# Kernel optimization log

Hardware: AMD Instinct MI355X
Metric: run time of the kernel (lower is better)

## Reference

```python
import jax, jax.numpy as jnp
import numpy as np

C = 80           # foreground classes
B, N = 8, 4000   # images, proposals per image
K_PRE = 2048     # pre-NMS candidates per image (fixed-shape stand-in for torch.where filtering)
DET = 100        # detection_per_image
SCORE_THRESH = 0.01
NMS_THRESH = 0.5
MIN_AREA = 0.1
BBOX_W = (10.0, 10.0, 5.0, 5.0)
CLIP = float(np.log(1000.0 / 16.0))
CLS_OFFSET = 4096.0               # > max image coordinate, for batched (per-class) NMS


def setup_inputs() -> dict:
    key = jax.random.key(0)
    k1, k2, k3, k4 = jax.random.split(key, 4)
    p1 = jax.random.uniform(k1, (B, N, 2)) * 800.0
    wh = jax.random.uniform(k2, (B, N, 2)) * 200.0 + 1.0
    proposals = jnp.concatenate([p1, p1 + wh], axis=-1)          # [B,N,4] x1,y1,x2,y2
    label_pre = jax.random.normal(k3, (B, N, C + 1), dtype=jnp.float32)
    bbox_pre = jax.random.normal(k4, (B, N, (C + 1) * 4), dtype=jnp.float32) * 0.5
    return {"label_pre": label_pre, "bbox_pre": bbox_pre, "proposals": proposals}


def decode_boxes(deltas, props):
    w = props[..., 2] - props[..., 0]
    h = props[..., 3] - props[..., 1]
    cx = props[..., 0] + 0.5 * w
    cy = props[..., 1] + 0.5 * h
    dx = deltas[..., 0] / BBOX_W[0]
    dy = deltas[..., 1] / BBOX_W[1]
    dw = jnp.minimum(deltas[..., 2] / BBOX_W[2], CLIP)
    dh = jnp.minimum(deltas[..., 3] / BBOX_W[3], CLIP)
    pcx = dx * w + cx
    pcy = dy * h + cy
    pw = jnp.exp(dw) * w
    ph = jnp.exp(dh) * h
    return jnp.stack([pcx - 0.5 * pw, pcy - 0.5 * ph,
                      pcx + 0.5 * pw, pcy + 0.5 * ph], axis=-1)


def pairwise_iou(b):
    # b [K,4] -> [K,K]
    area = jnp.maximum(b[:, 2] - b[:, 0], 0.0) * jnp.maximum(b[:, 3] - b[:, 1], 0.0)
    lt = jnp.maximum(b[:, None, :2], b[None, :, :2])
    rb = jnp.minimum(b[:, None, 2:], b[None, :, 2:])
    wh = jnp.maximum(rb - lt, 0.0)
    inter = wh[..., 0] * wh[..., 1]
    union = area[:, None] + area[None, :] - inter
    return inter / jnp.maximum(union, 1e-9)


def greedy_nms_keep(boxes, valid):
    # boxes already sorted by score (descending); returns kept mask
    K = boxes.shape[0]
    iou = pairwise_iou(boxes)
    idx = jnp.arange(K)

    def body(i, keep):
        sup = (iou[i] > NMS_THRESH) & (idx > i) & keep[i]
        return keep & ~sup

    return jax.lax.fori_loop(0, K, body, valid)


def process_image(logits, deltas, props):
    probs = jax.nn.softmax(logits, axis=-1)            # [N, C+1]
    scores = probs[:, 1:].reshape(-1)                  # [N*C]
    d = deltas[:, 4:].reshape(N, C, 4)                 # drop background deltas
    boxes = decode_boxes(d, props[:, None, :]).reshape(-1, 4)   # [N*C, 4]
    labels = jnp.broadcast_to(jnp.arange(1, C + 1), (N, C)).reshape(-1)
    area = (boxes[:, 3] - boxes[:, 1]) * (boxes[:, 2] - boxes[:, 0])
    valid = (scores > SCORE_THRESH) & (area > MIN_AREA)
    masked = jnp.where(valid, scores, -1.0)
    top_scores, top_idx = jax.lax.top_k(masked, K_PRE)
    top_boxes = boxes[top_idx]
    top_labels = labels[top_idx]
    keep0 = top_scores > 0.0
    # batched_nms: per-class coordinate offset so classes never suppress each other
    off = (top_labels.astype(top_boxes.dtype) * CLS_OFFSET)[:, None]
    keep = greedy_nms_keep(top_boxes + off, keep0)
    final = jnp.where(keep, top_scores, -1.0)
    det_scores, det_idx = jax.lax.top_k(final, DET)
    return top_boxes[det_idx], det_scores, top_labels[det_idx]


def reference(label_pre, bbox_pre, proposals):
    # returns (boxes [B,DET,4], scores [B,DET], labels [B,DET]); entries with score<0 are padding
    return jax.vmap(process_image)(label_pre, bbox_pre, proposals)
```

## Files before the change

### kernel.cpp

```cpp
#include <hip/hip_runtime.h>
#include <stdint.h>

#define B_ 8
#define N_ 4000
#define C_ 80
#define NC_ (N_ * C_)
#define KP_ 2048
#define CAND_ 4096
#define SLOTS_ 32
#define SLOTCAP_ 128
#define DET_ 100
#define NW_ 32
#define CLIP_ 4.135166556742356f

#define PB_ 80
#define IB_ (N_ / PB_)
#define CB_ 64
#define FB_ 128
#define NBLK_ ((NC_ / 4 + 255) / 256)

#define RT_ 256
#define RI_ 4
#define RJS_ 16
#define RSL_ (CAND_ / RJS_)
#define RIB_ (CAND_ / (RT_ * RI_))
#define IBK_ (CAND_ / 256)

typedef unsigned long long u64;

__device__ __forceinline__ void decode4(const float4 pr, const float4 d,
                                        float& x1, float& y1, float& x2, float& y2) {
  float w = pr.z - pr.x, h = pr.w - pr.y;
  float cx = pr.x + 0.5f * w, cy = pr.y + 0.5f * h;
  float dx = d.x / 10.0f, dy = d.y / 10.0f;
  float dw = fminf(d.z / 5.0f, CLIP_), dh = fminf(d.w / 5.0f, CLIP_);
  float pcx = dx * w + cx, pcy = dy * h + cy;
  float pw = expf(dw) * w, ph = expf(dh) * h;
  x1 = pcx - 0.5f * pw; y1 = pcy - 0.5f * ph;
  x2 = pcx + 0.5f * pw; y2 = pcy + 0.5f * ph;
}

__global__ __launch_bounds__(256) void k_scores(const float* __restrict__ logits,
                                                uint32_t* __restrict__ keys,
                                                uint32_t* __restrict__ imgHist) {
  __shared__ float lds[PB_ * 81];
  __shared__ float mArr[PB_], dArr[PB_];
  __shared__ uint32_t hcnt[CB_];
  int blk = blockIdx.x;
  int b = blk / IB_, lb = blk - b * IB_;
  int p0 = b * N_ + lb * PB_;
  int t = threadIdx.x;
  if (t < CB_) hcnt[t] = 0;
  const float4* src = (const float4*)(logits + (size_t)p0 * 81);
  for (int k = t; k < PB_ * 81 / 4; k += 256) ((float4*)lds)[k] = src[k];
  __syncthreads();
  if (t < PB_) {
    const float* lp = lds + t * 81;
    float m = lp[0];
    for (int i = 1; i <= C_; ++i) m = fmaxf(m, lp[i]);
    float denom = 0.f;
    for (int i = 0; i <= C_; ++i) denom += expf(lp[i] - m);
    mArr[t] = m; dArr[t] = denom;
  }
  __syncthreads();
#pragma unroll
  for (int iter = 0; iter < PB_ * C_ / 256; ++iter) {
    int e = iter * 256 + t;
    int pp = e / C_, c = e - pp * C_;
    float lv = lds[pp * 81 + c + 1];
    float score = expf(lv - mArr[pp]) / dArr[pp];
    uint32_t key = 0;
    if (score > 0.01f) {
      key = __float_as_uint(score);
      atomicAdd(&hcnt[(key >> 20) - 960], 1u);
    }
    keys[(size_t)p0 * C_ + e] = key;
  }
  __syncthreads();
  if (t < CB_ && hcnt[t]) atomicAdd(&imgHist[b * CB_ + t], hcnt[t]);
}

__global__ __launch_bounds__(256) void k_refine(const uint32_t* __restrict__ keys,
                                                const uint32_t* __restrict__ imgHist,
                                                uint32_t* __restrict__ fineHist) {
  __shared__ int s_cb;
  int blk = blockIdx.x;
  int b = blk / NBLK_, lb = blk - b * NBLK_;
  int t = threadIdx.x;
  if (t < 64) {
    uint32_t v = imgHist[b * CB_ + t];
#pragma unroll
    for (int d = 1; d < 64; d <<= 1) {
      uint32_t o = __shfl_down(v, d);
      v += (t + d < 64) ? o : 0;
    }
    uint32_t nxt = __shfl_down(v, 1);
    if (t == 63) nxt = 0;
    uint32_t total = __shfl(v, 0);
    if (t == 0 && total < KP_) s_cb = -1;
    if (total >= KP_ && v >= KP_ && nxt < KP_) s_cb = t;
  }
  __syncthreads();
  int cb = s_cb;
  if (cb < 0) return;
  int ti = lb * 256 + t;
  if (ti >= NC_ / 4) return;
  uint4 k4 = ((const uint4*)(keys + (size_t)b * NC_))[ti];
  uint32_t want = (uint32_t)(cb + 960);
  uint32_t kv[4] = {k4.x, k4.y, k4.z, k4.w};
#pragma unroll
  for (int q = 0; q < 4; ++q)
    if ((kv[q] >> 20) == want)
      atomicAdd(&fineHist[b * FB_ + ((kv[q] >> 13) & (FB_ - 1))], 1u);
}

__global__ __launch_bounds__(256) void k_compact(const uint32_t* __restrict__ keys,
                                                 const uint32_t* __restrict__ imgHist,
                                                 const uint32_t* __restrict__ fineHist,
                                                 uint32_t* __restrict__ cnt,
                                                 u64* __restrict__ cand) {
  __shared__ int s_cb;
  __shared__ uint32_t s_tail;
  __shared__ uint32_t s_thr;
  int blk = blockIdx.x;
  int b = blk / NBLK_, lb = blk - b * NBLK_;
  int t = threadIdx.x;
  if (t < 64) {
    uint32_t v = imgHist[b * CB_ + t];
#pragma unroll
    for (int d = 1; d < 64; d <<= 1) {
      uint32_t o = __shfl_down(v, d);
      v += (t + d < 64) ? o : 0;
    }
    uint32_t nxt = __shfl_down(v, 1);
    if (t == 63) nxt = 0;
    uint32_t total = __shfl(v, 0);
    if (t == 0 && total < KP_) { s_cb = -1; s_tail = 0; }
    if (total >= KP_ && v >= KP_ && nxt < KP_) { s_cb = t; s_tail = nxt; }
  }
  __syncthreads();
  int cb = s_cb;
  if (cb < 0) {
    if (t == 0) s_thr = 1u;
  } else if (t < 64) {
    uint32_t f0 = fineHist[b * FB_ + 2 * t];
    uint32_t f1 = fineHist[b * FB_ + 2 * t + 1];
    uint32_t v = f0 + f1;
#pragma unroll
    for (int d = 1; d < 64; d <<= 1) {
      uint32_t o = __shfl_down(v, d);
      v += (t + d < 64) ? o : 0;
    }
    uint32_t nxt = __shfl_down(v, 1);
    if (t == 63) nxt = 0;
    uint32_t tail = s_tail;
    bool c0 = (tail + v >= KP_);
    bool c1 = (tail + nxt + f1 >= KP_);
    bool cN = (tail + nxt >= KP_);
    if (c0 && !c1) s_thr = ((uint32_t)(cb + 960) << 20) | ((uint32_t)(2 * t) << 13);
    if (c1 && !cN) s_thr = ((uint32_t)(cb + 960) << 20) | ((uint32_t)(2 * t + 1) << 13);
  }
  __syncthreads();
  uint32_t thrb = s_thr;
  int ti = lb * 256 + t;
  if (ti >= NC_ / 4) return;
  uint4 k4 = ((const uint4*)(keys + (size_t)b * NC_))[ti];
  int slot = (ti >> 4) & (SLOTS_ - 1);
  uint32_t kv[4] = {k4.x, k4.y, k4.z, k4.w};
  int ns = 0;
#pragma unroll
  for (int q = 0; q < 4; ++q) ns += (kv[q] >= thrb) ? 1 : 0;
  if (ns == 0) return;
  uint32_t pos = atomicAdd(&cnt[(b * SLOTS_ + slot) * 16], (uint32_t)ns);
  u64* seg = cand + (size_t)b * CAND_ + slot * SLOTCAP_;
  uint32_t baseIdx = (uint32_t)(ti * 4);
#pragma unroll
  for (int q = 0; q < 4; ++q) {
    if (kv[q] >= thrb) {
      if (pos < SLOTCAP_)
        seg[pos] = ((u64)kv[q] << 32) | (uint32_t)(~(baseIdx + q));
      ++pos;
    }
  }
}

__global__ __launch_bounds__(256) void k_rank(const u64* __restrict__ cand,
                                              uint32_t* __restrict__ rankPart) {
  __shared__ u64 sh[RSL_];
  int blk = blockIdx.x;
  int b = blk / (RIB_ * RJS_);
  int rem = blk - b * (RIB_ * RJS_);
  int lb = rem / RJS_, js = rem - lb * RJS_;
  int t = threadIdx.x;
  const u64* cb2 = cand + (size_t)b * CAND_;
  if (t < RSL_ / 2)
    ((ulonglong2*)sh)[t] = ((const ulonglong2*)(cb2 + js * RSL_))[t];
  int base = lb * (RT_ * RI_) + t;
  u64 ki[RI_];
#pragma unroll
  for (int q = 0; q < RI_; ++q) ki[q] = cb2[base + q * RT_];
  __syncthreads();
  int cnt[RI_] = {0, 0, 0, 0};
#pragma unroll 4
  for (int j2 = 0; j2 < RSL_ / 2; ++j2) {
    ulonglong2 v = ((const ulonglong2*)sh)[j2];
#pragma unroll
    for (int q = 0; q < RI_; ++q) {
      cnt[q] += (v.x > ki[q]) ? 1 : 0;
      cnt[q] += (v.y > ki[q]) ? 1 : 0;
    }
  }
  uint32_t* rp = rankPart + ((size_t)(b * RJS_ + js)) * CAND_ + base;
#pragma unroll
  for (int q = 0; q < RI_; ++q) rp[q * RT_] = (uint32_t)cnt[q];
}

__global__ __launch_bounds__(256) void k_scatter(
    const u64* __restrict__ cand, const uint32_t* __restrict__ rankPart,
    const float* __restrict__ bbox, const float* __restrict__ props,
    float* __restrict__ topScore, int* __restrict__ topLabel,
    float* __restrict__ topBox, float* __restrict__ nmsBox) {
  int blk = blockIdx.x;
  int b = blk / IBK_, lb = blk - b * IBK_;
  int t = threadIdx.x;
  int i = lb * 256 + t;
  u64 ki = cand[(size_t)b * CAND_ + i];
  if (ki == 0ull) return;
  uint32_t r = 0;
#pragma unroll
  for (int js = 0; js < RJS_; ++js)
    r += rankPart[((size_t)(b * RJS_ + js)) * CAND_ + i];
  if (r >= KP_) return;
  uint32_t sbits = (uint32_t)(ki >> 32);
  uint32_t idx = ~((uint32_t)ki);
  int n = idx / C_, c = idx % C_;
  float4 pr4 = ((const float4*)props)[(size_t)b * N_ + n];
  float4 d = ((const float4*)(bbox + ((size_t)b * N_ + n) * ((C_ + 1) * 4)))[c + 1];
  float x1, y1, x2, y2;
  decode4(pr4, d, x1, y1, x2, y2);
  float off = (float)(c + 1) * 4096.0f;
  size_t o = (size_t)b * KP_ + (size_t)r;
  topScore[o] = __uint_as_float(sbits);
  topLabel[o] = c + 1;
  ((float4*)topBox)[o] = make_float4(x1, y1, x2, y2);
  ((float4*)nmsBox)[o] = make_float4(x1 + off, y1 + off, x2 + off, y2 + off);
}

__global__ __launch_bounds__(64) void k_supmat(const float* __restrict__ nmsBox,
                                               u64* __restrict__ sup) {
  int blk = blockIdx.x;
  int b = blk / 528, r = blk - b * 528;
  int ti = 0, rem = r;
  while (rem >= 32 - ti) { rem -= 32 - ti; ++ti; }
  int tj = ti + rem;
  __shared__ float4 shj[64];
  __shared__ float sha[64];
  int l = threadIdx.x;
  const float4* boxes = (const float4*)(nmsBox + (size_t)b * KP_ * 4);
  float4 bj0 = boxes[tj * 64 + l];
  shj[l] = bj0;
  sha[l] = fmaxf(bj0.z - bj0.x, 0.f) * fmaxf(bj0.w - bj0.y, 0.f);
  int i = ti * 64 + l;
  float4 bi = boxes[i];
  float areai = fmaxf(bi.z - bi.x, 0.f) * fmaxf(bi.w - bi.y, 0.f);
  __syncthreads();
  u64 bits = 0;
  for (int jj = 0; jj < 64; ++jj) {
    int j = tj * 64 + jj;
    if (j > i) {
      float4 bj = shj[jj];
      float ltx = fmaxf(bi.x, bj.x), lty = fmaxf(bi.y, bj.y);
      float rbx = fminf(bi.z, bj.z), rby = fminf(bi.w, bj.w);
      float iw = fmaxf(rbx - ltx, 0.f), ih = fmaxf(rby - lty, 0.f);
      float inter = iw * ih;
      float uni = areai + sha[jj] - inter;
      float iou = inter / fmaxf(uni, 1e-9f);
      if (iou > 0.5f) bits |= (1ull << jj);
    }
  }
  sup[((size_t)b * KP_ + i) * NW_ + tj] = bits;
}

__global__ __launch_bounds__(64) void k_nms_scan(const u64* __restrict__ sup,
                                                 const float* __restrict__ topScore,
                                                 const int* __restrict__ topLabel,
                                                 const float* __restrict__ topBox,
                                                 float* __restrict__ out) {
  int b = blockIdx.x, l = threadIdx.x;
  int h = l >> 5, w = l & 31;
  const u64* base = sup + (size_t)b * KP_ * NW_;
  const float* ts = topScore + (size_t)b * KP_;
  const int* tl = topLabel + (size_t)b * KP_;
  const float4* tb = (const float4*)(topBox + (size_t)b * KP_ * 4);
  unsigned m32 = 0;
#pragma unroll
  for (int j = 0; j < 8; ++j) {
    float4 s4 = ((const float4*)ts)[l * 8 + j];
    if (!(s4.x > 0.f)) m32 |= 1u << (4 * j + 0);
// ... 47 lines not shown
      emitRow(c * 64 + k, true);
    }
    if (outCount >= DET_) return true;
    unsigned kmask = h ? ~rmh : ~rml;
    u64 acc = 0;
#pragma unroll
    for (int k = 0; k < 32; ++k)
      acc |= ((kmask >> k) & 1u) ? cur[k] : 0ull;
    acc |= __shfl_xor(acc, 32);
    removed = (l == c) ? rmfull : removed;
    if (l < 32 && l >= c) removed |= acc;
    return false;
  };

  bool done = false;
  loadc(ra, 0);
  for (int c = 0; c < NW_ && !done; c += 2) {
    if (c + 1 < NW_) loadc(rb, c + 1);
    done = chunk(ra, c);
    if (!done) {
      if (c + 2 < NW_) loadc(ra, c + 2);
      done = chunk(rb, c + 1);
    }
  }
  if (outCount < DET_) {
    for (int c2 = 0; c2 < NW_ && outCount < DET_; ++c2) {
      u64 rm = __shfl(removed, c2);
      while (rm && outCount < DET_) {
        int k = __builtin_ctzll(rm);
        rm &= rm - 1;
        emitRow(c2 * 64 + k, false);
      }
    }
  }
}

extern "C" void kernel_launch(void* const* d_in, const int* in_sizes, int n_in,
                              void* d_out, int out_size, void* d_ws, size_t ws_size,
                              hipStream_t stream) {
  const float* label_pre = (const float*)d_in[0];
  const float* bbox_pre = (const float*)d_in[1];
  const float* props = (const float*)d_in[2];
  float* out = (float*)d_out;

  char* ws = (char*)d_ws;
  size_t off = 0;
  auto alloc = [&](size_t bytes) -> void* {
    void* p = ws + off;
    off = (off + bytes + 255) & ~(size_t)255;
    return p;
  };

  uint32_t* keys = (uint32_t*)alloc((size_t)B_ * NC_ * 4);
  size_t zero_begin = off;
  uint32_t* imgHist = (uint32_t*)alloc((size_t)B_ * CB_ * 4);
  uint32_t* fineHist = (uint32_t*)alloc((size_t)B_ * FB_ * 4);
  uint32_t* cnt = (uint32_t*)alloc((size_t)B_ * SLOTS_ * 16 * 4);
  u64* cand = (u64*)alloc((size_t)B_ * CAND_ * 8);
  float* topScore = (float*)alloc((size_t)B_ * KP_ * 4);
  int* topLabel = (int*)alloc((size_t)B_ * KP_ * 4);
  float* topBox = (float*)alloc((size_t)B_ * KP_ * 16);
  float* nmsBox = (float*)alloc((size_t)B_ * KP_ * 16);
  size_t zero_end = off;
  u64* sup = (u64*)alloc((size_t)B_ * KP_ * NW_ * 8);
  uint32_t* rankPart = (uint32_t*)alloc((size_t)B_ * RJS_ * CAND_ * 4);

  if (off > ws_size) return;

  hipMemsetAsync(ws + zero_begin, 0, zero_end - zero_begin, stream);

  k_scores<<<B_ * IB_, 256, 0, stream>>>(label_pre, keys, imgHist);
  k_refine<<<B_ * NBLK_, 256, 0, stream>>>(keys, imgHist, fineHist);
  k_compact<<<B_ * NBLK_, 256, 0, stream>>>(keys, imgHist, fineHist, cnt, cand);
  k_rank<<<B_ * RIB_ * RJS_, RT_, 0, stream>>>(cand, rankPart);
  k_scatter<<<B_ * IBK_, 256, 0, stream>>>(cand, rankPart, bbox_pre, props,
                                           topScore, topLabel, topBox, nmsBox);
  k_supmat<<<B_ * 528, 64, 0, stream>>>(nmsBox, sup);
  k_nms_scan<<<B_, 64, 0, stream>>>(sup, topScore, topLabel, topBox, out);
}
```

Measured before the change: 183.7 us.

## Fuse all pipeline stages into one cooperative persistent kernel with grid syncs

Replaces the memset plus seven separate kernel launches with a single cooperative kernel of 512 blocks that runs each stage in turn, separated by grid-wide barriers. Zeroing of the workspace happens inside the kernel. The goal is to remove per-launch overhead and the gaps between dependent kernels. In exchange, each stage is limited to the fixed grid, and the supmat and refine/compact stages become grid-stride loops. Grid syncs have their own cost, and if the cooperative launch fails the old multi-kernel path runs instead.

```diff
diff --git a/kernel.cpp b/kernel.cpp
--- a/kernel.cpp
+++ b/kernel.cpp
@@ -1,5 +1,8 @@
 #include <hip/hip_runtime.h>
+#include <hip/hip_cooperative_groups.h>
 #include <stdint.h>
+
+namespace cg = cooperative_groups;
 
 #define B_ 8
 #define N_ 4000
@@ -26,6 +29,8 @@
 #define RIB_ (CAND_ / (RT_ * RI_))
 #define IBK_ (CAND_ / 256)
 
+#define GB_ 512
+
 typedef unsigned long long u64;
 
 __device__ __forceinline__ void decode4(const float4 pr, const float4 d,
@@ -38,6 +43,358 @@
   float pw = expf(dw) * w, ph = expf(dh) * h;
   x1 = pcx - 0.5f * pw; y1 = pcy - 0.5f * ph;
   x2 = pcx + 0.5f * pw; y2 = pcy + 0.5f * ph;
+}
+
+struct SmScores { float lds[PB_ * 81]; float mArr[PB_]; float dArr[PB_]; uint32_t hcnt[CB_]; };
+struct SmSel { int s_cb; uint32_t s_tail; uint32_t s_thr; };
+struct SmSup { float4 shj[4][64]; float sha[4][64]; };
+union SmAll { SmScores sc; SmSel sel; u64 rk[RSL_]; SmSup sup; };
+
+__global__ __launch_bounds__(256, 2) void k_mega(
+    const float* __restrict__ logits, const float* __restrict__ bbox,
+    const float* __restrict__ props,
+    uint32_t* __restrict__ keys, uint32_t* __restrict__ imgHist,
+    uint32_t* __restrict__ fineHist, uint32_t* __restrict__ cnt,
+    u64* __restrict__ cand, float* __restrict__ topScore,
+    int* __restrict__ topLabel, float* __restrict__ topBox,
+    float* __restrict__ nmsBox, u64* __restrict__ sup,
+    uint32_t* __restrict__ rankPart, float* __restrict__ out,
+    uint4* __restrict__ zeroPtr, int zeroN4) {
+  cg::grid_group grid = cg::this_grid();
+  __shared__ SmAll sm;
+  int bid = blockIdx.x, t = threadIdx.x;
+
+  for (int i = bid * 256 + t; i < zeroN4; i += GB_ * 256)
+    zeroPtr[i] = make_uint4(0u, 0u, 0u, 0u);
+  grid.sync();
+
+  if (bid < B_ * IB_) {
+    int b = bid / IB_, lb = bid - b * IB_;
+    int p0 = b * N_ + lb * PB_;
+    if (t < CB_) sm.sc.hcnt[t] = 0;
+    const float4* src = (const float4*)(logits + (size_t)p0 * 81);
+    for (int k = t; k < PB_ * 81 / 4; k += 256) ((float4*)sm.sc.lds)[k] = src[k];
+    __syncthreads();
+    if (t < PB_) {
+      const float* lp = sm.sc.lds + t * 81;
+      float m = lp[0];
+      for (int i = 1; i <= C_; ++i) m = fmaxf(m, lp[i]);
+      float denom = 0.f;
+      for (int i = 0; i <= C_; ++i) denom += expf(lp[i] - m);
+      sm.sc.mArr[t] = m; sm.sc.dArr[t] = denom;
+    }
+    __syncthreads();
+#pragma unroll
+    for (int iter = 0; iter < PB_ * C_ / 256; ++iter) {
+      int e = iter * 256 + t;
+      int pp = e / C_, c = e - pp * C_;
+      float lv = sm.sc.lds[pp * 81 + c + 1];
+      float score = expf(lv - sm.sc.mArr[pp]) / sm.sc.dArr[pp];
+      uint32_t key = 0;
+      if (score > 0.01f) {
+        key = __float_as_uint(score);
+        atomicAdd(&sm.sc.hcnt[(key >> 20) - 960], 1u);
+      }
+      keys[(size_t)p0 * C_ + e] = key;
+    }
+    __syncthreads();
+    if (t < CB_ && sm.sc.hcnt[t]) atomicAdd(&imgHist[b * CB_ + t], sm.sc.hcnt[t]);
+  }
+  grid.sync();
+
+  for (int vb = bid; vb < B_ * NBLK_; vb += GB_) {
+    __syncthreads();
+    int b = vb / NBLK_, lb = vb - b * NBLK_;
+    if (t < 64) {
+      uint32_t v = imgHist[b * CB_ + t];
+#pragma unroll
+      for (int d = 1; d < 64; d <<= 1) {
+        uint32_t o = __shfl_down(v, d);
+        v += (t + d < 64) ? o : 0;
+      }
+      uint32_t nxt = __shfl_down(v, 1);
+      if (t == 63) nxt = 0;
+      uint32_t total = __shfl(v, 0);
+      if (t == 0 && total < KP_) sm.sel.s_cb = -1;
+      if (total >= KP_ && v >= KP_ && nxt < KP_) sm.sel.s_cb = t;
+    }
+    __syncthreads();
+    int cb = sm.sel.s_cb;
+    if (cb >= 0) {
+      int ti = lb * 256 + t;
+      if (ti < NC_ / 4) {
+        uint4 k4 = ((const uint4*)(keys + (size_t)b * NC_))[ti];
+        uint32_t want = (uint32_t)(cb + 960);
+        uint32_t kv[4] = {k4.x, k4.y, k4.z, k4.w};
+#pragma unroll
+        for (int q = 0; q < 4; ++q)
+          if ((kv[q] >> 20) == want)
+            atomicAdd(&fineHist[b * FB_ + ((kv[q] >> 13) & (FB_ - 1))], 1u);
+      }
+    }
+  }
+  grid.sync();
+
+  for (int vb = bid; vb < B_ * NBLK_; vb += GB_) {
+    __syncthreads();
+    int b = vb / NBLK_, lb = vb - b * NBLK_;
+    if (t < 64) {
+      uint32_t v = imgHist[b * CB_ + t];
+#pragma unroll
+      for (int d = 1; d < 64; d <<= 1) {
+        uint32_t o = __shfl_down(v, d);
+        v += (t + d < 64) ? o : 0;
+      }
+      uint32_t nxt = __shfl_down(v, 1);
+      if (t == 63) nxt = 0;
+      uint32_t total = __shfl(v, 0);
+      if (t == 0 && total < KP_) { sm.sel.s_cb = -1; sm.sel.s_tail = 0; }
+      if (total >= KP_ && v >= KP_ && nxt < KP_) { sm.sel.s_cb = t; sm.sel.s_tail = nxt; }
+    }
+    __syncthreads();
+    int cb = sm.sel.s_cb;
+    if (cb < 0) {
+      if (t == 0) sm.sel.s_thr = 1u;
+    } else if (t < 64) {
+      uint32_t f0 = fineHist[b * FB_ + 2 * t];
+      uint32_t f1 = fineHist[b * FB_ + 2 * t + 1];
+      uint32_t v = f0 + f1;
+#pragma unroll
+      for (int d = 1; d < 64; d <<= 1) {
+        uint32_t o = __shfl_down(v, d);
+        v += (t + d < 64) ? o : 0;
+      }
+      uint32_t nxt = __shfl_down(v, 1);
+      if (t == 63) nxt = 0;
+      uint32_t tail = sm.sel.s_tail;
+      bool c0 = (tail + v >= KP_);
+      bool c1 = (tail + nxt + f1 >= KP_);
+      bool cN = (tail + nxt >= KP_);
+      if (c0 && !c1) sm.sel.s_thr = ((uint32_t)(cb + 960) << 20) | ((uint32_t)(2 * t) << 13);
+      if (c1 && !cN) sm.sel.s_thr = ((uint32_t)(cb + 960) << 20) | ((uint32_t)(2 * t + 1) << 13);
+    }
+    __syncthreads();
+    uint32_t thrb = sm.sel.s_thr;
+    int ti = lb * 256 + t;
+    if (ti < NC_ / 4) {
+      uint4 k4 = ((const uint4*)(keys + (size_t)b * NC_))[ti];
+      int slot = (ti >> 4) & (SLOTS_ - 1);
+      uint32_t kv[4] = {k4.x, k4.y, k4.z, k4.w};
+      int ns = 0;
+#pragma unroll
+      for (int q = 0; q < 4; ++q) ns += (kv[q] >= thrb) ? 1 : 0;
+      if (ns != 0) {
+        uint32_t pos = atomicAdd(&cnt[(b * SLOTS_ + slot) * 16], (uint32_t)ns);
+        u64* seg = cand + (size_t)b * CAND_ + slot * SLOTCAP_;
+        uint32_t baseIdx = (uint32_t)(ti * 4);
+#pragma unroll
+        for (int q = 0; q < 4; ++q) {
+          if (kv[q] >= thrb) {
+            if (pos < SLOTCAP_)
+              seg[pos] = ((u64)kv[q] << 32) | (uint32_t)(~(baseIdx + q));
+            ++pos;
+          }
+        }
+      }
+    }
+  }
+  grid.sync();
+
+  {
+    int b = bid / (RIB_ * RJS_);
+    int rem = bid - b * (RIB_ * RJS_);
+    int lb = rem / RJS_, js = rem - lb * RJS_;
+    const u64* cb2 = cand + (size_t)b * CAND_;
+    if (t < RSL_ / 2)
+      ((ulonglong2*)sm.rk)[t] = ((const ulonglong2*)(cb2 + js * RSL_))[t];
+    int base = lb * (RT_ * RI_) + t;
+    u64 ki[RI_];
+#pragma unroll
+    for (int q = 0; q < RI_; ++q) ki[q] = cb2[base + q * RT_];
+    __syncthreads();
+    int cnt4[RI_] = {0, 0, 0, 0};
+#pragma unroll 4
+    for (int j2 = 0; j2 < RSL_ / 2; ++j2) {
+      ulonglong2 v = ((const ulonglong2*)sm.rk)[j2];
+#pragma unroll
+      for (int q = 0; q < RI_; ++q) {
+        cnt4[q] += (v.x > ki[q]) ? 1 : 0;
+        cnt4[q] += (v.y > ki[q]) ? 1 : 0;
+      }
+    }
+    uint32_t* rp = rankPart + ((size_t)(b * RJS_ + js)) * CAND_ + base;
+#pragma unroll
+    for (int q = 0; q < RI_; ++q) rp[q * RT_] = (uint32_t)cnt4[q];
+  }
+  grid.sync();
+
+  if (bid < B_ * IBK_) {
+    int b = bid / IBK_, lb = bid - b * IBK_;
+    int i = lb * 256 + t;
+    u64 ki = cand[(size_t)b * CAND_ + i];
+    if (ki != 0ull) {
+      uint32_t r = 0;
+#pragma unroll
+      for (int js = 0; js < RJS_; ++js)
+        r += rankPart[((size_t)(b * RJS_ + js)) * CAND_ + i];
+      if (r < KP_) {
+        uint32_t sbits = (uint32_t)(ki >> 32);
+        uint32_t idx = ~((uint32_t)ki);
+        int n = idx / C_, c = idx % C_;
+        float4 pr4 = ((const float4*)props)[(size_t)b * N_ + n];
+        float4 d = ((const float4*)(bbox + ((size_t)b * N_ + n) * ((C_ + 1) * 4)))[c + 1];
+        float x1, y1, x2, y2;
+        decode4(pr4, d, x1, y1, x2, y2);
+        float off = (float)(c + 1) * 4096.0f;
+        size_t o = (size_t)b * KP_ + (size_t)r;
+        topScore[o] = __uint_as_float(sbits);
+        topLabel[o] = c + 1;
+        ((float4*)topBox)[o] = make_float4(x1, y1, x2, y2);
+        ((float4*)nmsBox)[o] = make_float4(x1 + off, y1 + off, x2 + off, y2 + off);
+      }
+    }
+  }
+  grid.sync();
+
+  {
+    int l = t & 63, wv = t >> 6;
+    for (int pass = 0; pass < (B_ * 528 + GB_ * 4 - 1) / (GB_ * 4); ++pass) {
+      int tt = pass * GB_ * 4 + bid * 4 + wv;
+      bool act = tt < B_ * 528;
+      int b = 0, tj = 0, i = 0;
+      float4 bi = make_float4(0.f, 0.f, 0.f, 0.f);
+      float areai = 0.f;
+      __syncthreads();
+      if (act) {
+        b = tt / 528;
+        int r = tt - b * 528;
+        int ti2 = 0, rem2 = r;
+        while (rem2 >= 32 - ti2) { rem2 -= 32 - ti2; ++ti2; }
+        tj = ti2 + rem2;
+        const float4* boxes = (const float4*)(nmsBox + (size_t)b * KP_ * 4);
+        float4 bj0 = boxes[tj * 64 + l];
+        sm.sup.shj[wv][l] = bj0;
+        sm.sup.sha[wv][l] = fmaxf(bj0.z - bj0.x, 0.f) * fmaxf(bj0.w - bj0.y, 0.f);
+        i = ti2 * 64 + l;
+        bi = boxes[i];
+        areai = fmaxf(bi.z - bi.x, 0.f) * fmaxf(bi.w - bi.y, 0.f);
+      }
+      __syncthreads();
+      if (act) {
+        u64 bits = 0;
+        for (int jj = 0; jj < 64; ++jj) {
+          int j = tj * 64 + jj;
+          if (j > i) {
+            float4 bj = sm.sup.shj[wv][jj];
+            float ltx = fmaxf(bi.x, bj.x), lty = fmaxf(bi.y, bj.y);
+            float rbx = fminf(bi.z, bj.z), rby = fminf(bi.w, bj.w);
+            float iw = fmaxf(rbx - ltx, 0.f), ih = fmaxf(rby - lty, 0.f);
+            float inter = iw * ih;
+            float uni = areai + sm.sup.sha[wv][jj] - inter;
+            float iou = inter / fmaxf(uni, 1e-9f);
+            if (iou > 0.5f) bits |= (1ull << jj);
+          }
+        }
+        sup[((size_t)b * KP_ + i) * NW_ + tj] = bits;
+      }
+    }
+  }
+  grid.sync();
+
+  if (bid < B_ && t < 64) {
+    int b = bid, l = t;
+    int h = l >> 5, w = l & 31;
+    const u64* base = sup + (size_t)b * KP_ * NW_;
+    const float* ts = topScore + (size_t)b * KP_;
+    const int* tl = topLabel + (size_t)b * KP_;
+    const float4* tb = (const float4*)(topBox + (size_t)b * KP_ * 4);
+    unsigned m32 = 0;
+#pragma unroll
+    for (int j = 0; j < 8; ++j) {
+      float4 s4 = ((const float4*)ts)[l * 8 + j];
+      if (!(s4.x > 0.f)) m32 |= 1u << (4 * j + 0);
+      if (!(s4.y > 0.f)) m32 |= 1u << (4 * j + 1);
+      if (!(s4.z > 0.f)) m32 |= 1u << (4 * j + 2);
+      if (!(s4.w > 0.f)) m32 |= 1u << (4 * j + 3);
+    }
+    u64 removed = ((u64)__shfl(m32, 2 * w + 1) << 32) | (u64)__shfl(m32, 2 * w);
+
+    int outCount = 0;
+    auto emitRow = [&](int row, bool kept) {
+      if (l == (outCount & 63)) {
+        float4 bx = tb[row];
+        out[((size_t)b * DET_ + outCount) * 4 + 0] = bx.x;
+        out[((size_t)b * DET_ + outCount) * 4 + 1] = bx.y;
+        out[((size_t)b * DET_ + outCount) * 4 + 2] = bx.z;
+        out[((size_t)b * DET_ + outCount) * 4 + 3] = bx.w;
+        out[B_ * DET_ * 4 + (size_t)b * DET_ + outCount] = kept ? ts[row] : -1.0f;
+        out[B_ * DET_ * 4 + B_ * DET_ + (size_t)b * DET_ + outCount] = (float)tl[row];
+      }
+      ++outCount;
+    };
+
+    u64 ra[32], rb[32];
+    auto loadc = [&](u64* dst, int c) {
+      const u64* p = base + ((size_t)c * 64 + h * 32) * NW_ + w;
+#pragma unroll
+      for (int k = 0; k < 32; ++k) dst[k] = p[(size_t)k * NW_];
+    };
+    auto chunk = [&](u64* cur, int c) -> bool {
+      u64 rm = __shfl(removed, c);
+      unsigned rml = (unsigned)rm, rmh = (unsigned)(rm >> 32);
+#pragma unroll
+      for (int k = 0; k < 32; ++k) {
+        unsigned dlo = __builtin_amdgcn_readlane((unsigned)cur[k], c);
+        unsigned dhi = __builtin_amdgcn_readlane((unsigned)(cur[k] >> 32), c);
+        if (!((rml >> k) & 1u)) { rml |= dlo; rmh |= dhi; }
+      }
+#pragma unroll
+      for (int k = 0; k < 32; ++k) {
+        unsigned dlo = __builtin_amdgcn_readlane((unsigned)cur[k], 32 + c);
+        unsigned dhi = __builtin_amdgcn_readlane((unsigned)(cur[k] >> 32), 32 + c);
+        if (!((rmh >> k) & 1u)) { rml |= dlo; rmh |= dhi; }
+      }
+      u64 rmfull = ((u64)rmh << 32) | rml;
+      u64 kb = ~rmfull;
+      while (kb) {
+        if (outCount >= DET_) return true;
+        int k = __builtin_ctzll(kb);
+        kb &= kb - 1;
+        emitRow(c * 64 + k, true);
+      }
+      if (outCount >= DET_) return true;
+      unsigned kmask = h ? ~rmh : ~rml;
+      u64 acc = 0;
+#pragma unroll
+      for (int k = 0; k < 32; ++k)
+        acc |= ((kmask >> k) & 1u) ? cur[k] : 0ull;
+      acc |= __shfl_xor(acc, 32);
+      removed = (l == c) ? rmfull : removed;
+      if (l < 32 && l >= c) removed |= acc;
+      return false;
+    };
+
+    bool done = false;
+    loadc(ra, 0);
+    for (int c = 0; c < NW_ && !done; c += 2) {
+      if (c + 1 < NW_) loadc(rb, c + 1);
+      done = chunk(ra, c);
+      if (!done) {
+        if (c + 2 < NW_) loadc(ra, c + 2);
+        done = chunk(rb, c + 1);
+      }
+    }
+    if (outCount < DET_) {
+      for (int c2 = 0; c2 < NW_ && outCount < DET_; ++c2) {
+        u64 rm = __shfl(removed, c2);
+        while (rm && outCount < DET_) {
+          int k = __builtin_ctzll(rm);
+          rm &= rm - 1;
+          emitRow(c2 * 64 + k, false);
+        }
+      }
+    }
+  }
 }
 
 __global__ __launch_bounds__(256) void k_scores(const float* __restrict__ logits,
@@ -200,19 +557,19 @@
 #pragma unroll
   for (int q = 0; q < RI_; ++q) ki[q] = cb2[base + q * RT_];
   __syncthreads();
-  int cnt[RI_] = {0, 0, 0, 0};
+  int cnt4[RI_] = {0, 0, 0, 0};
 #pragma unroll 4
   for (int j2 = 0; j2 < RSL_ / 2; ++j2) {
     ulonglong2 v = ((const ulonglong2*)sh)[j2];
 #pragma unroll
     for (int q = 0; q < RI_; ++q) {
-      cnt[q] += (v.x > ki[q]) ? 1 : 0;
-      cnt[q] += (v.y > ki[q]) ? 1 : 0;
+      cnt4[q] += (v.x > ki[q]) ? 1 : 0;
+      cnt4[q] += (v.y > ki[q]) ? 1 : 0;
     }
   }
   uint32_t* rp = rankPart + ((size_t)(b * RJS_ + js)) * CAND_ + base;
 #pragma unroll
-  for (int q = 0; q < RI_; ++q) rp[q * RT_] = (uint32_t)cnt[q];
+  for (int q = 0; q < RI_; ++q) rp[q * RT_] = (uint32_t)cnt4[q];
 }
 
 __global__ __launch_bounds__(256) void k_scatter(
@@ -412,14 +769,26 @@
 
   if (off > ws_size) return;
 
-  hipMemsetAsync(ws + zero_begin, 0, zero_end - zero_begin, stream);
-
-  k_scores<<<B_ * IB_, 256, 0, stream>>>(label_pre, keys, imgHist);
-  k_refine<<<B_ * NBLK_, 256, 0, stream>>>(keys, imgHist, fineHist);
-  k_compact<<<B_ * NBLK_, 256, 0, stream>>>(keys, imgHist, fineHist, cnt, cand);
-  k_rank<<<B_ * RIB_ * RJS_, RT_, 0, stream>>>(cand, rankPart);
-  k_scatter<<<B_ * IBK_, 256, 0, stream>>>(cand, rankPart, bbox_pre, props,
-                                           topScore, topLabel, topBox, nmsBox);
-  k_supmat<<<B_ * 528, 64, 0, stream>>>(nmsBox, sup);
-  k_nms_scan<<<B_, 64, 0, stream>>>(sup, topScore, topLabel, topBox, out);
-}
+  uint4* zeroPtr = (uint4*)(ws + zero_begin);
+  int zeroN4 = (int)((zero_end - zero_begin) / 16);
+
+  void* kargs[] = {
+      (void*)&label_pre, (void*)&bbox_pre, (void*)&props,
+      (void*)&keys, (void*)&imgHist, (void*)&fineHist, (void*)&cnt,
+      (void*)&cand, (void*)&topScore, (void*)&topLabel, (void*)&topBox,
+      (void*)&nmsBox, (void*)&sup, (void*)&rankPart, (void*)&out,
+      (void*)&zeroPtr, (void*)&zeroN4};
+  hipError_t err = hipLaunchCooperativeKernel((const void*)k_mega, dim3(GB_),
+                                              dim3(256), kargs, 0, stream);
+  if (err != hipSuccess) {
+    hipMemsetAsync(ws + zero_begin, 0, zero_end - zero_begin, stream);
+    k_scores<<<B_ * IB_, 256, 0, stream>>>(label_pre, keys, imgHist);
+    k_refine<<<B_ * NBLK_, 256, 0, stream>>>(keys, imgHist, fineHist);
+    k_compact<<<B_ * NBLK_, 256, 0, stream>>>(keys, imgHist, fineHist, cnt, cand);
+    k_rank<<<B_ * RIB_ * RJS_, RT_, 0, stream>>>(cand, rankPart);
+    k_scatter<<<B_ * IBK_, 256, 0, stream>>>(cand, rankPart, bbox_pre, props,
+                                             topScore, topLabel, topBox, nmsBox);
+    k_supmat<<<B_ * 528, 64, 0, stream>>>(nmsBox, sup);
+    k_nms_scan<<<B_, 64, 0, stream>>>(sup, topScore, topLabel, topBox, out);
+  }
+}
```

Result: slower. 557.7 us (+203.6%).

## Single-pass fine histogram, fuse scatter into rank via last-block ticket

Applied to the files above, without the earlier changes.

Replaces the two-level coarse/refine histogram with one fine 6912-bin global histogram built directly in the score kernel, which removes the k_refine pass over all keys. The threshold search now runs inside k_compact. The scatter kernel is folded into k_rank: the last block per image, chosen by an atomic ticket, does the rank summation and decode. Zeroing of the candidate and top buffers moves from memset into the kernels, and the score kernel uses smaller blocks. The cost is heavier global atomic contention on the fine histogram and a serialized scatter done by one block per image.

```diff
diff --git a/kernel.cpp b/kernel.cpp
--- a/kernel.cpp
+++ b/kernel.cpp
@@ -13,18 +13,19 @@
 #define NW_ 32
 #define CLIP_ 4.135166556742356f
 
-#define PB_ 80
+#define PB_ 16
 #define IB_ (N_ / PB_)
-#define CB_ 64
-#define FB_ 128
 #define NBLK_ ((NC_ / 4 + 255) / 256)
+
+#define NBIN_ 6912
+#define BINBASE_ 123136u
 
 #define RT_ 256
 #define RI_ 4
 #define RJS_ 16
 #define RSL_ (CAND_ / RJS_)
 #define RIB_ (CAND_ / (RT_ * RI_))
-#define IBK_ (CAND_ / 256)
+#define RNB_ (RIB_ * RJS_)
 
 typedef unsigned long long u64;
 
@@ -42,15 +43,16 @@
 
 __global__ __launch_bounds__(256) void k_scores(const float* __restrict__ logits,
                                                 uint32_t* __restrict__ keys,
-                                                uint32_t* __restrict__ imgHist) {
+                                                uint32_t* __restrict__ fineHist,
+                                                uint4* __restrict__ zcc, int zccN) {
   __shared__ float lds[PB_ * 81];
   __shared__ float mArr[PB_], dArr[PB_];
-  __shared__ uint32_t hcnt[CB_];
   int blk = blockIdx.x;
   int b = blk / IB_, lb = blk - b * IB_;
   int p0 = b * N_ + lb * PB_;
   int t = threadIdx.x;
-  if (t < CB_) hcnt[t] = 0;
+  for (int i = blk * 256 + t; i < zccN; i += B_ * IB_ * 256)
+    zcc[i] = make_uint4(0u, 0u, 0u, 0u);
   const float4* src = (const float4*)(logits + (size_t)p0 * 81);
   for (int k = t; k < PB_ * 81 / 4; k += 256) ((float4*)lds)[k] = src[k];
   __syncthreads();
@@ -72,93 +74,52 @@
     uint32_t key = 0;
     if (score > 0.01f) {
       key = __float_as_uint(score);
-      atomicAdd(&hcnt[(key >> 20) - 960], 1u);
+      atomicAdd(&fineHist[b * NBIN_ + ((key >> 13) - BINBASE_)], 1u);
     }
     keys[(size_t)p0 * C_ + e] = key;
   }
-  __syncthreads();
-  if (t < CB_ && hcnt[t]) atomicAdd(&imgHist[b * CB_ + t], hcnt[t]);
-}
-
-__global__ __launch_bounds__(256) void k_refine(const uint32_t* __restrict__ keys,
-                                                const uint32_t* __restrict__ imgHist,
-                                                uint32_t* __restrict__ fineHist) {
-  __shared__ int s_cb;
-  int blk = blockIdx.x;
-  int b = blk / NBLK_, lb = blk - b * NBLK_;
-  int t = threadIdx.x;
-  if (t < 64) {
-    uint32_t v = imgHist[b * CB_ + t];
-#pragma unroll
-    for (int d = 1; d < 64; d <<= 1) {
-      uint32_t o = __shfl_down(v, d);
-      v += (t + d < 64) ? o : 0;
-    }
-    uint32_t nxt = __shfl_down(v, 1);
-    if (t == 63) nxt = 0;
-    uint32_t total = __shfl(v, 0);
-    if (t == 0 && total < KP_) s_cb = -1;
-    if (total >= KP_ && v >= KP_ && nxt < KP_) s_cb = t;
-  }
-  __syncthreads();
-  int cb = s_cb;
-  if (cb < 0) return;
-  int ti = lb * 256 + t;
-  if (ti >= NC_ / 4) return;
-  uint4 k4 = ((const uint4*)(keys + (size_t)b * NC_))[ti];
-  uint32_t want = (uint32_t)(cb + 960);
-  uint32_t kv[4] = {k4.x, k4.y, k4.z, k4.w};
-#pragma unroll
-  for (int q = 0; q < 4; ++q)
-    if ((kv[q] >> 20) == want)
-      atomicAdd(&fineHist[b * FB_ + ((kv[q] >> 13) & (FB_ - 1))], 1u);
 }
 
 __global__ __launch_bounds__(256) void k_compact(const uint32_t* __restrict__ keys,
-                                                 const uint32_t* __restrict__ imgHist,
                                                  const uint32_t* __restrict__ fineHist,
                                                  uint32_t* __restrict__ cnt,
-                                                 u64* __restrict__ cand) {
-  __shared__ int s_cb;
-  __shared__ uint32_t s_tail;
+                                                 u64* __restrict__ cand,
+                                                 uint4* __restrict__ ztop, int ztopN) {
+  __shared__ uint32_t wtot[4];
   __shared__ uint32_t s_thr;
   int blk = blockIdx.x;
   int b = blk / NBLK_, lb = blk - b * NBLK_;
   int t = threadIdx.x;
-  if (t < 64) {
-    uint32_t v = imgHist[b * CB_ + t];
-#pragma unroll
-    for (int d = 1; d < 64; d <<= 1) {
-      uint32_t o = __shfl_down(v, d);
-      v += (t + d < 64) ? o : 0;
-    }
-    uint32_t nxt = __shfl_down(v, 1);
-    if (t == 63) nxt = 0;
-    uint32_t total = __shfl(v, 0);
-    if (t == 0 && total < KP_) { s_cb = -1; s_tail = 0; }
-    if (total >= KP_ && v >= KP_ && nxt < KP_) { s_cb = t; s_tail = nxt; }
-  }
-  __syncthreads();
-  int cb = s_cb;
-  if (cb < 0) {
-    if (t == 0) s_thr = 1u;
-  } else if (t < 64) {
-    uint32_t f0 = fineHist[b * FB_ + 2 * t];
-    uint32_t f1 = fineHist[b * FB_ + 2 * t + 1];
-    uint32_t v = f0 + f1;
-#pragma unroll
-    for (int d = 1; d < 64; d <<= 1) {
-      uint32_t o = __shfl_down(v, d);
-      v += (t + d < 64) ? o : 0;
-    }
-    uint32_t nxt = __shfl_down(v, 1);
-    if (t == 63) nxt = 0;
-    uint32_t tail = s_tail;
-    bool c0 = (tail + v >= KP_);
-    bool c1 = (tail + nxt + f1 >= KP_);
-    bool cN = (tail + nxt >= KP_);
-    if (c0 && !c1) s_thr = ((uint32_t)(cb + 960) << 20) | ((uint32_t)(2 * t) << 13);
-    if (c1 && !cN) s_thr = ((uint32_t)(cb + 960) << 20) | ((uint32_t)(2 * t + 1) << 13);
+  int lane = t & 63, wv = t >> 6;
+  for (int i = blk * 256 + t; i < ztopN; i += B_ * NBLK_ * 256)
+    ztop[i] = make_uint4(0u, 0u, 0u, 0u);
+  const uint32_t* fh = fineHist + b * NBIN_ + t * 27;
+  uint32_t csum = 0;
+#pragma unroll
+  for (int j = 0; j < 27; ++j) csum += fh[j];
+  uint32_t v = csum;
+#pragma unroll
+  for (int d = 1; d < 64; d <<= 1) {
+    uint32_t o = __shfl_down(v, d);
+    v += (lane + d < 64) ? o : 0;
+  }
+  if (lane == 0) wtot[wv] = v;
+  __syncthreads();
+  uint32_t hi = 0;
+  for (int w2 = wv + 1; w2 < 4; ++w2) hi += wtot[w2];
+  uint32_t suffInc = v + hi;
+  uint32_t suffExc = suffInc - csum;
+  uint32_t total = wtot[0] + wtot[1] + wtot[2] + wtot[3];
+  if (t == 0 && total < KP_) s_thr = 1u;
+  if (total >= KP_ && suffInc >= KP_ && suffExc < KP_) {
+    uint32_t running = suffExc;
+    for (int j = 26; j >= 0; --j) {
+      running += fh[j];
+      if (running >= KP_) {
+        s_thr = (BINBASE_ + (uint32_t)t * 27u + (uint32_t)j) << 13;
+        break;
+      }
+    }
   }
   __syncthreads();
   uint32_t thrb = s_thr;
@@ -184,12 +145,17 @@
   }
 }
 
-__global__ __launch_bounds__(256) void k_rank(const u64* __restrict__ cand,
-                                              uint32_t* __restrict__ rankPart) {
+__global__ __launch_bounds__(256) void k_rank(
+    const u64* __restrict__ cand, uint32_t* __restrict__ rankPart,
+    uint32_t* __restrict__ ticket,
+    const float* __restrict__ bbox, const float* __restrict__ props,
+    float* __restrict__ topScore, int* __restrict__ topLabel,
+    float* __restrict__ topBox, float* __restrict__ nmsBox) {
   __shared__ u64 sh[RSL_];
+  __shared__ uint32_t s_old;
   int blk = blockIdx.x;
-  int b = blk / (RIB_ * RJS_);
-  int rem = blk - b * (RIB_ * RJS_);
+  int b = blk / RNB_;
+  int rem = blk - b * RNB_;
   int lb = rem / RJS_, js = rem - lb * RJS_;
   int t = threadIdx.x;
   const u64* cb2 = cand + (size_t)b * CAND_;
@@ -200,50 +166,49 @@
 #pragma unroll
   for (int q = 0; q < RI_; ++q) ki[q] = cb2[base + q * RT_];
   __syncthreads();
-  int cnt[RI_] = {0, 0, 0, 0};
+  int cnt4[RI_] = {0, 0, 0, 0};
 #pragma unroll 4
   for (int j2 = 0; j2 < RSL_ / 2; ++j2) {
     ulonglong2 v = ((const ulonglong2*)sh)[j2];
 #pragma unroll
     for (int q = 0; q < RI_; ++q) {
-      cnt[q] += (v.x > ki[q]) ? 1 : 0;
-      cnt[q] += (v.y > ki[q]) ? 1 : 0;
+      cnt4[q] += (v.x > ki[q]) ? 1 : 0;
+      cnt4[q] += (v.y > ki[q]) ? 1 : 0;
     }
   }
   uint32_t* rp = rankPart + ((size_t)(b * RJS_ + js)) * CAND_ + base;
 #pragma unroll
-  for (int q = 0; q < RI_; ++q) rp[q * RT_] = (uint32_t)cnt[q];
-}
-
-__global__ __launch_bounds__(256) void k_scatter(
-    const u64* __restrict__ cand, const uint32_t* __restrict__ rankPart,
-    const float* __restrict__ bbox, const float* __restrict__ props,
-    float* __restrict__ topScore, int* __restrict__ topLabel,
-    float* __restrict__ topBox, float* __restrict__ nmsBox) {
-  int blk = blockIdx.x;
-  int b = blk / IBK_, lb = blk - b * IBK_;
-  int t = threadIdx.x;
-  int i = lb * 256 + t;
-  u64 ki = cand[(size_t)b * CAND_ + i];
-  if (ki == 0ull) return;
-  uint32_t r = 0;
-#pragma unroll
-  for (int js = 0; js < RJS_; ++js)
-    r += rankPart[((size_t)(b * RJS_ + js)) * CAND_ + i];
-  if (r >= KP_) return;
-  uint32_t sbits = (uint32_t)(ki >> 32);
-  uint32_t idx = ~((uint32_t)ki);
-  int n = idx / C_, c = idx % C_;
-  float4 pr4 = ((const float4*)props)[(size_t)b * N_ + n];
-  float4 d = ((const float4*)(bbox + ((size_t)b * N_ + n) * ((C_ + 1) * 4)))[c + 1];
-  float x1, y1, x2, y2;
-  decode4(pr4, d, x1, y1, x2, y2);
-  float off = (float)(c + 1) * 4096.0f;
-  size_t o = (size_t)b * KP_ + (size_t)r;
-  topScore[o] = __uint_as_float(sbits);
-  topLabel[o] = c + 1;
-  ((float4*)topBox)[o] = make_float4(x1, y1, x2, y2);
-  ((float4*)nmsBox)[o] = make_float4(x1 + off, y1 + off, x2 + off, y2 + off);
+  for (int q = 0; q < RI_; ++q) rp[q * RT_] = (uint32_t)cnt4[q];
+
+  __threadfence();
+  __syncthreads();
+  if (t == 0) s_old = atomicAdd(&ticket[b], 1u);
+  __syncthreads();
+  if (s_old == RNB_ - 1) {
+    __threadfence();
+    for (int i = t; i < CAND_; i += RT_) {
+      u64 kk = cb2[i];
+      if (kk == 0ull) continue;
+      uint32_t r = 0;
+#pragma unroll
+      for (int js2 = 0; js2 < RJS_; ++js2)
+        r += rankPart[((size_t)(b * RJS_ + js2)) * CAND_ + i];
+      if (r >= KP_) continue;
+      uint32_t sbits = (uint32_t)(kk >> 32);
+      uint32_t idx = ~((uint32_t)kk);
+      int n = idx / C_, c = idx % C_;
+      float4 pr4 = ((const float4*)props)[(size_t)b * N_ + n];
+      float4 d = ((const float4*)(bbox + ((size_t)b * N_ + n) * ((C_ + 1) * 4)))[c + 1];
+      float x1, y1, x2, y2;
+      decode4(pr4, d, x1, y1, x2, y2);
+      float off = (float)(c + 1) * 4096.0f;
+      size_t o = (size_t)b * KP_ + (size_t)r;
+      topScore[o] = __uint_as_float(sbits);
+      topLabel[o] = c + 1;
+      ((float4*)topBox)[o] = make_float4(x1, y1, x2, y2);
+      ((float4*)nmsBox)[o] = make_float4(x1 + off, y1 + off, x2 + off, y2 + off);
+    }
+  }
 }
 
 __global__ __launch_bounds__(64) void k_supmat(const float* __restrict__ nmsBox,
@@ -398,28 +363,31 @@
 
   uint32_t* keys = (uint32_t*)alloc((size_t)B_ * NC_ * 4);
   size_t zero_begin = off;
-  uint32_t* imgHist = (uint32_t*)alloc((size_t)B_ * CB_ * 4);
-  uint32_t* fineHist = (uint32_t*)alloc((size_t)B_ * FB_ * 4);
+  uint32_t* fineHist = (uint32_t*)alloc((size_t)B_ * NBIN_ * 4);
+  uint32_t* ticket = (uint32_t*)alloc((size_t)B_ * 4);
+  size_t zero_end = off;
   uint32_t* cnt = (uint32_t*)alloc((size_t)B_ * SLOTS_ * 16 * 4);
   u64* cand = (u64*)alloc((size_t)B_ * CAND_ * 8);
   float* topScore = (float*)alloc((size_t)B_ * KP_ * 4);
   int* topLabel = (int*)alloc((size_t)B_ * KP_ * 4);
   float* topBox = (float*)alloc((size_t)B_ * KP_ * 16);
   float* nmsBox = (float*)alloc((size_t)B_ * KP_ * 16);
-  size_t zero_end = off;
   u64* sup = (u64*)alloc((size_t)B_ * KP_ * NW_ * 8);
   uint32_t* rankPart = (uint32_t*)alloc((size_t)B_ * RJS_ * CAND_ * 4);
 
   if (off > ws_size) return;
 
+  uint4* zcc = (uint4*)cnt;
+  int zccN = (int)(((size_t)B_ * SLOTS_ * 16 * 4 + (size_t)B_ * CAND_ * 8) / 16);
+  uint4* ztop = (uint4*)topScore;
+  int ztopN = (int)(((size_t)B_ * KP_ * 4 * 2 + (size_t)B_ * KP_ * 16 * 2) / 16);
+
   hipMemsetAsync(ws + zero_begin, 0, zero_end - zero_begin, stream);
 
-  k_scores<<<B_ * IB_, 256, 0, stream>>>(label_pre, keys, imgHist);
-  k_refine<<<B_ * NBLK_, 256, 0, stream>>>(keys, imgHist, fineHist);
-  k_compact<<<B_ * NBLK_, 256, 0, stream>>>(keys, imgHist, fineHist, cnt, cand);
-  k_rank<<<B_ * RIB_ * RJS_, RT_, 0, stream>>>(cand, rankPart);
-  k_scatter<<<B_ * IBK_, 256, 0, stream>>>(cand, rankPart, bbox_pre, props,
-                                           topScore, topLabel, topBox, nmsBox);
+  k_scores<<<B_ * IB_, 256, 0, stream>>>(label_pre, keys, fineHist, zcc, zccN);
+  k_compact<<<B_ * NBLK_, 256, 0, stream>>>(keys, fineHist, cnt, cand, ztop, ztopN);
+  k_rank<<<B_ * RNB_, RT_, 0, stream>>>(cand, rankPart, ticket, bbox_pre, props,
+                                        topScore, topLabel, topBox, nmsBox);
   k_supmat<<<B_ * 528, 64, 0, stream>>>(nmsBox, sup);
   k_nms_scan<<<B_, 64, 0, stream>>>(sup, topScore, topLabel, topBox, out);
 }
```

Measured after the change: 316.8 us. +72.5%, slower.

## Fold workspace zeroing into score kernel and use per-block partial histograms

Applied to the files above, without the earlier changes.

Drops the hipMemsetAsync and zeroes the workspace inside k_scores. The global coarse-histogram atomics become per-block partial histograms, which the refine and compact kernels sum themselves. The score kernel now uses smaller blocks (16 proposals instead of 80) for more parallelism. The refine and compact kernels each process 5 uint4 per thread across 64 blocks per image, and refine accumulates its fine histogram in LDS first. This removes a memset launch and reduces global atomic contention, at the cost of every refine/compact block redundantly reading all 250 partial histograms for its image.

```diff
diff --git a/kernel.cpp b/kernel.cpp
--- a/kernel.cpp
+++ b/kernel.cpp
@@ -13,11 +13,12 @@
 #define NW_ 32
 #define CLIP_ 4.135166556742356f
 
-#define PB_ 80
+#define PB_ 16
 #define IB_ (N_ / PB_)
 #define CB_ 64
 #define FB_ 128
-#define NBLK_ ((NC_ / 4 + 255) / 256)
+#define SEGB_ 64
+#define U4PT_ 5
 
 #define RT_ 256
 #define RI_ 4
@@ -40,9 +41,21 @@
   x2 = pcx + 0.5f * pw; y2 = pcy + 0.5f * ph;
 }
 
+__device__ __forceinline__ uint32_t coarse_sum(const uint32_t* __restrict__ histPart,
+                                               int b, int t, uint32_t (*wsum)[CB_]) {
+  int l = t & 63, wv = t >> 6;
+  uint32_t v = 0;
+  for (int j = wv; j < IB_; j += 4)
+    v += histPart[((size_t)b * IB_ + j) * CB_ + l];
+  wsum[wv][l] = v;
+  __syncthreads();
+  return (t < CB_) ? (wsum[0][t] + wsum[1][t] + wsum[2][t] + wsum[3][t]) : 0u;
+}
+
 __global__ __launch_bounds__(256) void k_scores(const float* __restrict__ logits,
                                                 uint32_t* __restrict__ keys,
-                                                uint32_t* __restrict__ imgHist) {
+                                                uint32_t* __restrict__ histPart,
+                                                uint4* __restrict__ zr, int zrN) {
   __shared__ float lds[PB_ * 81];
   __shared__ float mArr[PB_], dArr[PB_];
   __shared__ uint32_t hcnt[CB_];
@@ -50,6 +63,8 @@
   int b = blk / IB_, lb = blk - b * IB_;
   int p0 = b * N_ + lb * PB_;
   int t = threadIdx.x;
+  for (int i = blk * 256 + t; i < zrN; i += B_ * IB_ * 256)
+    zr[i] = make_uint4(0u, 0u, 0u, 0u);
   if (t < CB_) hcnt[t] = 0;
   const float4* src = (const float4*)(logits + (size_t)p0 * 81);
   for (int k = t; k < PB_ * 81 / 4; k += 256) ((float4*)lds)[k] = src[k];
@@ -77,18 +92,22 @@
     keys[(size_t)p0 * C_ + e] = key;
   }
   __syncthreads();
-  if (t < CB_ && hcnt[t]) atomicAdd(&imgHist[b * CB_ + t], hcnt[t]);
+  if (t < CB_) histPart[((size_t)b * IB_ + lb) * CB_ + t] = hcnt[t];
 }
 
 __global__ __launch_bounds__(256) void k_refine(const uint32_t* __restrict__ keys,
-                                                const uint32_t* __restrict__ imgHist,
+                                                const uint32_t* __restrict__ histPart,
                                                 uint32_t* __restrict__ fineHist) {
+  __shared__ uint32_t wsum[4][CB_];
   __shared__ int s_cb;
-  int blk = blockIdx.x;
-  int b = blk / NBLK_, lb = blk - b * NBLK_;
+  __shared__ uint32_t hf[FB_];
+  int blk = blockIdx.x;
+  int b = blk / SEGB_, lb = blk - b * SEGB_;
   int t = threadIdx.x;
-  if (t < 64) {
-    uint32_t v = imgHist[b * CB_ + t];
+  if (t < FB_) hf[t] = 0;
+  uint32_t cv = coarse_sum(histPart, b, t, wsum);
+  if (t < CB_) {
+    uint32_t v = cv;
 #pragma unroll
     for (int d = 1; d < 64; d <<= 1) {
       uint32_t o = __shfl_down(v, d);
@@ -103,30 +122,39 @@
   __syncthreads();
   int cb = s_cb;
   if (cb < 0) return;
-  int ti = lb * 256 + t;
-  if (ti >= NC_ / 4) return;
-  uint4 k4 = ((const uint4*)(keys + (size_t)b * NC_))[ti];
   uint32_t want = (uint32_t)(cb + 960);
-  uint32_t kv[4] = {k4.x, k4.y, k4.z, k4.w};
-#pragma unroll
-  for (int q = 0; q < 4; ++q)
-    if ((kv[q] >> 20) == want)
-      atomicAdd(&fineHist[b * FB_ + ((kv[q] >> 13) & (FB_ - 1))], 1u);
+  const uint4* kp4 = (const uint4*)(keys + (size_t)b * NC_);
+#pragma unroll
+  for (int q = 0; q < U4PT_; ++q) {
+    int ti = lb * (256 * U4PT_) + q * 256 + t;
+    if (ti < NC_ / 4) {
+      uint4 k4 = kp4[ti];
+      uint32_t kv[4] = {k4.x, k4.y, k4.z, k4.w};
+#pragma unroll
+      for (int qq = 0; qq < 4; ++qq)
+        if ((kv[qq] >> 20) == want)
+          atomicAdd(&hf[(kv[qq] >> 13) & (FB_ - 1)], 1u);
+    }
+  }
+  __syncthreads();
+  if (t < FB_ && hf[t]) atomicAdd(&fineHist[b * FB_ + t], hf[t]);
 }
 
 __global__ __launch_bounds__(256) void k_compact(const uint32_t* __restrict__ keys,
-                                                 const uint32_t* __restrict__ imgHist,
+                                                 const uint32_t* __restrict__ histPart,
                                                  const uint32_t* __restrict__ fineHist,
                                                  uint32_t* __restrict__ cnt,
                                                  u64* __restrict__ cand) {
+  __shared__ uint32_t wsum[4][CB_];
   __shared__ int s_cb;
   __shared__ uint32_t s_tail;
   __shared__ uint32_t s_thr;
   int blk = blockIdx.x;
-  int b = blk / NBLK_, lb = blk - b * NBLK_;
+  int b = blk / SEGB_, lb = blk - b * SEGB_;
   int t = threadIdx.x;
-  if (t < 64) {
-    uint32_t v = imgHist[b * CB_ + t];
+  uint32_t cv = coarse_sum(histPart, b, t, wsum);
+  if (t < CB_) {
+    uint32_t v = cv;
 #pragma unroll
     for (int d = 1; d < 64; d <<= 1) {
       uint32_t o = __shfl_down(v, d);
@@ -162,24 +190,28 @@
   }
   __syncthreads();
   uint32_t thrb = s_thr;
-  int ti = lb * 256 + t;
-  if (ti >= NC_ / 4) return;
-  uint4 k4 = ((const uint4*)(keys + (size_t)b * NC_))[ti];
-  int slot = (ti >> 4) & (SLOTS_ - 1);
-  uint32_t kv[4] = {k4.x, k4.y, k4.z, k4.w};
-  int ns = 0;
-#pragma unroll
-  for (int q = 0; q < 4; ++q) ns += (kv[q] >= thrb) ? 1 : 0;
-  if (ns == 0) return;
-  uint32_t pos = atomicAdd(&cnt[(b * SLOTS_ + slot) * 16], (uint32_t)ns);
-  u64* seg = cand + (size_t)b * CAND_ + slot * SLOTCAP_;
-  uint32_t baseIdx = (uint32_t)(ti * 4);
-#pragma unroll
-  for (int q = 0; q < 4; ++q) {
-    if (kv[q] >= thrb) {
-      if (pos < SLOTCAP_)
-        seg[pos] = ((u64)kv[q] << 32) | (uint32_t)(~(baseIdx + q));
-      ++pos;
+  const uint4* kp4 = (const uint4*)(keys + (size_t)b * NC_);
+#pragma unroll
+  for (int q = 0; q < U4PT_; ++q) {
+    int ti = lb * (256 * U4PT_) + q * 256 + t;
+    if (ti >= NC_ / 4) break;
+    uint4 k4 = kp4[ti];
+    int slot = (ti >> 4) & (SLOTS_ - 1);
+    uint32_t kv[4] = {k4.x, k4.y, k4.z, k4.w};
+    int ns = 0;
+#pragma unroll
+    for (int qq = 0; qq < 4; ++qq) ns += (kv[qq] >= thrb) ? 1 : 0;
+    if (ns == 0) continue;
+    uint32_t pos = atomicAdd(&cnt[(b * SLOTS_ + slot) * 16], (uint32_t)ns);
+    u64* seg = cand + (size_t)b * CAND_ + slot * SLOTCAP_;
+    uint32_t baseIdx = (uint32_t)(ti * 4);
+#pragma unroll
+    for (int qq = 0; qq < 4; ++qq) {
+      if (kv[qq] >= thrb) {
+        if (pos < SLOTCAP_)
+          seg[pos] = ((u64)kv[qq] << 32) | (uint32_t)(~(baseIdx + qq));
+        ++pos;
+      }
     }
   }
 }
@@ -200,19 +232,19 @@
 #pragma unroll
   for (int q = 0; q < RI_; ++q) ki[q] = cb2[base + q * RT_];
   __syncthreads();
-  int cnt[RI_] = {0, 0, 0, 0};
+  int cnt4[RI_] = {0, 0, 0, 0};
 #pragma unroll 4
   for (int j2 = 0; j2 < RSL_ / 2; ++j2) {
     ulonglong2 v = ((const ulonglong2*)sh)[j2];
 #pragma unroll
     for (int q = 0; q < RI_; ++q) {
-      cnt[q] += (v.x > ki[q]) ? 1 : 0;
-      cnt[q] += (v.y > ki[q]) ? 1 : 0;
+      cnt4[q] += (v.x > ki[q]) ? 1 : 0;
+      cnt4[q] += (v.y > ki[q]) ? 1 : 0;
     }
   }
   uint32_t* rp = rankPart + ((size_t)(b * RJS_ + js)) * CAND_ + base;
 #pragma unroll
-  for (int q = 0; q < RI_; ++q) rp[q * RT_] = (uint32_t)cnt[q];
+  for (int q = 0; q < RI_; ++q) rp[q * RT_] = (uint32_t)cnt4[q];
 }
 
 __global__ __launch_bounds__(256) void k_scatter(
@@ -397,8 +429,8 @@
   };
 
   uint32_t* keys = (uint32_t*)alloc((size_t)B_ * NC_ * 4);
+  uint32_t* histPart = (uint32_t*)alloc((size_t)B_ * IB_ * CB_ * 4);
   size_t zero_begin = off;
-  uint32_t* imgHist = (uint32_t*)alloc((size_t)B_ * CB_ * 4);
   uint32_t* fineHist = (uint32_t*)alloc((size_t)B_ * FB_ * 4);
   uint32_t* cnt = (uint32_t*)alloc((size_t)B_ * SLOTS_ * 16 * 4);
   u64* cand = (u64*)alloc((size_t)B_ * CAND_ * 8);
@@ -412,11 +444,12 @@
 
   if (off > ws_size) return;
 
-  hipMemsetAsync(ws + zero_begin, 0, zero_end - zero_begin, stream);
-
-  k_scores<<<B_ * IB_, 256, 0, stream>>>(label_pre, keys, imgHist);
-  k_refine<<<B_ * NBLK_, 256, 0, stream>>>(keys, imgHist, fineHist);
-  k_compact<<<B_ * NBLK_, 256, 0, stream>>>(keys, imgHist, fineHist, cnt, cand);
+  uint4* zr = (uint4*)(ws + zero_begin);
+  int zrN = (int)((zero_end - zero_begin) / 16);
+
+  k_scores<<<B_ * IB_, 256, 0, stream>>>(label_pre, keys, histPart, zr, zrN);
+  k_refine<<<B_ * SEGB_, 256, 0, stream>>>(keys, histPart, fineHist);
+  k_compact<<<B_ * SEGB_, 256, 0, stream>>>(keys, histPart, fineHist, cnt, cand);
   k_rank<<<B_ * RIB_ * RJS_, RT_, 0, stream>>>(cand, rankPart);
   k_scatter<<<B_ * IBK_, 256, 0, stream>>>(cand, rankPart, bbox_pre, props,
                                            topScore, topLabel, topBox, nmsBox);
```

Result: slower. 193.7 us (+5.4%).
